# Kernel tuning notes

Measured on AMD Instinct MI355X. Metric: run time of the kernel, lower is better.

Reference implementation:

```python
import jax, jax.numpy as jnp
import numpy as np

N = 100000
DEG = 16
E = N * DEG
IN_DIM = 256
HID = 64
OUT = 64


def setup_inputs() -> dict:
    key = jax.random.key(0)
    ks = jax.random.split(key, 6)
    x = jax.random.normal(ks[0], (N, IN_DIM), dtype=jnp.float32)
    # CSR with fixed degree DEG: row i owns edges [i*DEG, (i+1)*DEG)
    row_id = jnp.repeat(jnp.arange(N, dtype=jnp.int64), DEG)
    col_id = jax.random.randint(ks[1], (E,), 0, N, dtype=jnp.int64)
    adj = jnp.stack([col_id, row_id])  # adj[0]=col, adj[1]=row (matches torch forward)
    row_ptr = (jnp.arange(N + 1, dtype=jnp.int64) * DEG)
    W1 = jax.random.normal(ks[2], (IN_DIM, HID), dtype=jnp.float32) / np.sqrt(IN_DIM)
    b1 = jnp.zeros((HID,), dtype=jnp.float32)
    W2 = jax.random.normal(ks[3], (HID, OUT), dtype=jnp.float32) / np.sqrt(HID)
    b2 = jnp.zeros((OUT,), dtype=jnp.float32)
    return {"x": x, "adj": adj, "row_ptr": row_ptr, "W1": W1, "b1": b1, "W2": W2, "b2": b2}


def agnn_layer(x, row, col, beta):
    # x: [N, d]; row/col: [E]. AGNN: e_ij = beta*cos(x_i, x_j), row-softmax, aggregate x_j.
    norm = jnp.maximum(jnp.linalg.norm(x, axis=-1, keepdims=True), 1e-12)
    xn = x / norm  # [N, d]
    e = beta * jnp.sum(xn[row] * xn[col], axis=-1)  # [E] cosine scores
    # numerically stable segment softmax over rows
    m = jax.ops.segment_max(e, row, num_segments=N)  # [N]
    ex = jnp.exp(e - m[row])  # [E]
    denom = jax.ops.segment_sum(ex, row, num_segments=N)  # [N]
    alpha = ex / jnp.maximum(denom[row], 1e-12)  # [E]
    out = jax.ops.segment_sum(alpha[:, None] * x[col], row, num_segments=N)  # [N, d]
    return out


def reference(x, adj, row_ptr, W1, b1, W2, b2):
    col, row = adj[0], adj[1]
    beta = jnp.float32(1.0)  # non-trainable buffer, initialized to ones
    h = jax.nn.relu(x @ W1 + b1)
    for _ in range(4):
        h = jax.nn.relu(agnn_layer(h, row, col, beta))
    return h @ W2 + b2
```

## Files before the change

kernel.cpp:

```cpp
#include <hip/hip_runtime.h>
#include <math.h>

#define N_NODES 100000
#define DEG 16
#define IN_DIM 256
#define HID 64

typedef _Float16 f16x8 __attribute__((ext_vector_type(8)));
typedef __fp16 fp16x2b __attribute__((ext_vector_type(2)));
typedef float f32x4 __attribute__((ext_vector_type(4)));

union F16x8u {
  f16x8 v;
  fp16x2b h2[4];
};

#if __has_builtin(__builtin_amdgcn_fdot2)
__device__ __forceinline__ float fdot2(fp16x2b a, fp16x2b b, float c) {
  return __builtin_amdgcn_fdot2(a, b, c, false);
}
#else
__device__ __forceinline__ float fdot2(fp16x2b a, fp16x2b b, float c) {
  return fmaf((float)a[0], (float)b[0], fmaf((float)a[1], (float)b[1], c));
}
#endif

__global__ __launch_bounds__(256) void extract_col_kernel(const int* __restrict__ adj,
                                                          int* __restrict__ col, int E) {
  const bool is64 = (adj[2 * E - 1] == 0);
  for (int e = blockIdx.x * blockDim.x + threadIdx.x; e < E; e += gridDim.x * blockDim.x) {
    col[e] = is64 ? adj[2 * e] : adj[e];
  }
}

__global__ __launch_bounds__(256) void prep_wfrag_kernel(const float* __restrict__ W,
                                                         _Float16* __restrict__ wfrag,
                                                         int nfrag) {
  const int id = blockIdx.x * 256 + threadIdx.x;
  if (id >= nfrag) return;
  const int lane = id & 63;
  const int nt = (id >> 6) & 3;
  const int kt = id >> 8;
  const int k0 = kt * 32 + (lane >> 4) * 8;
  const int c = nt * 16 + (lane & 15);
  f16x8 v;
#pragma unroll
  for (int j = 0; j < 8; ++j) v[j] = (_Float16)W[(k0 + j) * HID + c];
  ((f16x8*)wfrag)[id] = v;
}

__global__ __launch_bounds__(256) void mlp1_kernel(const float* __restrict__ x,
                                                   const _Float16* __restrict__ wfrag,
                                                   const float* __restrict__ b1,
                                                   _Float16* __restrict__ hn,
                                                   float* __restrict__ nrm) {
  __shared__ f16x8 Bs[2048];
#pragma unroll
  for (int i = 0; i < 8; ++i)
    Bs[threadIdx.x + 256 * i] = ((const f16x8*)wfrag)[threadIdx.x + 256 * i];

  const int lane = threadIdx.x & 63;
  const int wv = threadIdx.x >> 6;
  const int rbase = blockIdx.x * 64 + wv * 16;
  const int arow = min(rbase + (lane & 15), N_NODES - 1);
  const int kgrp = lane >> 4;
  const float* xrow = x + (size_t)arow * IN_DIM + kgrp * 8;

  f32x4 acc[4];
#pragma unroll
  for (int nt = 0; nt < 4; ++nt) acc[nt] = {0.0f, 0.0f, 0.0f, 0.0f};

  __syncthreads();

#pragma unroll
  for (int kt = 0; kt < 8; ++kt) {
    const float4 a0 = *(const float4*)&xrow[kt * 32];
    const float4 a1 = *(const float4*)&xrow[kt * 32 + 4];
    F16x8u u;
    u.h2[0] = __builtin_amdgcn_cvt_pkrtz(a0.x, a0.y);
    u.h2[1] = __builtin_amdgcn_cvt_pkrtz(a0.z, a0.w);
    u.h2[2] = __builtin_amdgcn_cvt_pkrtz(a1.x, a1.y);
    u.h2[3] = __builtin_amdgcn_cvt_pkrtz(a1.z, a1.w);
#pragma unroll
    for (int nt = 0; nt < 4; ++nt)
      acc[nt] = __builtin_amdgcn_mfma_f32_16x16x32_f16(u.v, Bs[(kt * 4 + nt) * 64 + lane],
                                                       acc[nt], 0, 0, 0);
  }

  const int colb = lane & 15;
  float bias[4];
#pragma unroll
  for (int nt = 0; nt < 4; ++nt) bias[nt] = b1[nt * 16 + colb];

#pragma unroll
  for (int j = 0; j < 4; ++j) {
    float o[4];
#pragma unroll
    for (int nt = 0; nt < 4; ++nt) o[nt] = fmaxf(acc[nt][j] + bias[nt], 0.0f);
    float ss = o[0] * o[0] + o[1] * o[1] + o[2] * o[2] + o[3] * o[3];
    ss += __shfl_xor(ss, 1); ss += __shfl_xor(ss, 2);
    ss += __shfl_xor(ss, 4); ss += __shfl_xor(ss, 8);
    const float nv = sqrtf(ss);
    const float inv = 1.0f / fmaxf(nv, 1e-12f);
    const int row = rbase + kgrp * 4 + j;
    if (row < N_NODES) {
#pragma unroll
      for (int nt = 0; nt < 4; ++nt)
        hn[(size_t)row * HID + nt * 16 + colb] = (_Float16)(o[nt] * inv);
      if (colb == 0) nrm[row] = nv;
    }
  }
}

__global__ __launch_bounds__(256) void agnn_kernel(const _Float16* __restrict__ hn,
                                                   const float* __restrict__ nrm,
                                                   const int* __restrict__ col,
                                                   _Float16* __restrict__ hn_out,
                                                   float* __restrict__ nrm_out) {
  const int lane = threadIdx.x & 63;
  const int wv = threadIdx.x >> 6;
  const int g = lane >> 3;
  const int q = lane & 7;
  const int node = blockIdx.x * 32 + wv * 8 + g;

  const f16x8* hp8 = (const f16x8*)hn;
  F16x8u xi;
  xi.v = hp8[(size_t)node * 8 + q];

  const int cidx0 = col[node * DEG + q];
  const int cidx1 = col[node * DEG + 8 + q];
  const float ncv0 = nrm[cidx0];
  const float ncv1 = nrm[cidx1];

  const int base = (lane & 56) * 4;

  float o[8];
#pragma unroll
  for (int d = 0; d < 8; ++d) o[d] = 0.0f;
  float dn = 0.0f;

#pragma unroll
  for (int c = 0; c < 2; ++c) {
    const int cs = c ? cidx1 : cidx0;
    const float ncv = c ? ncv1 : ncv0;

    F16x8u xcv[8];
#pragma unroll
    for (int k = 0; k < 8; ++k) {
      const int ce = __builtin_amdgcn_ds_bpermute(base + k * 4, cs);
      xcv[k].v = hp8[(size_t)((uint)ce) * 8u + (uint)q];
    }

    float t[8];
#pragma unroll
    for (int k = 0; k < 8; ++k) {
      float s = 0.0f;
#pragma unroll
      for (int j = 0; j < 4; ++j) s = fdot2(xi.h2[j], xcv[k].h2[j], s);
      t[k] = s;
    }

    const bool b0 = (lane & 1), b1 = (lane & 2), b2 = (lane & 4);
    float u[4];
#pragma unroll
    for (int j = 0; j < 4; ++j) {
      const float keep = b0 ? t[2 * j + 1] : t[2 * j];
      const float send = b0 ? t[2 * j] : t[2 * j + 1];
      u[j] = keep + __shfl_xor(send, 1);
    }
    float v[2];
#pragma unroll
    for (int j = 0; j < 2; ++j) {
      const float keep = b1 ? u[2 * j + 1] : u[2 * j];
      const float send = b1 ? u[2 * j] : u[2 * j + 1];
      v[j] = keep + __shfl_xor(send, 2);
    }
    float p;
    {
      const float keep = b2 ? v[1] : v[0];
      const float send = b2 ? v[0] : v[1];
      p = keep + __shfl_xor(send, 4);
    }

    const float ex = __expf(p);
    dn += ex;
    const float wgt = ex * ncv;

#pragma unroll
    for (int k = 0; k < 8; ++k) {
      const float wk = __int_as_float(
          __builtin_amdgcn_ds_bpermute(base + k * 4, __float_as_int(wgt)));
#pragma unroll
      for (int j = 0; j < 4; ++j) {
        o[2 * j] = fmaf((float)xcv[k].h2[j][0], wk, o[2 * j]);
        o[2 * j + 1] = fmaf((float)xcv[k].h2[j][1], wk, o[2 * j + 1]);
      }
    }
  }

  dn += __shfl_xor(dn, 1);
  dn += __shfl_xor(dn, 2);
  dn += __shfl_xor(dn, 4);
  const float idn = 1.0f / dn;

  float ss = 0.0f;
#pragma unroll
  for (int d = 0; d < 8; ++d) {
    o[d] = fmaxf(o[d] * idn, 0.0f);
    ss = fmaf(o[d], o[d], ss);
  }
  ss += __shfl_xor(ss, 1);
  ss += __shfl_xor(ss, 2);
  ss += __shfl_xor(ss, 4);
  const float nv = sqrtf(ss);
  const float inv = 1.0f / fmaxf(nv, 1e-12f);

  F16x8u ov;
#pragma unroll
  for (int d = 0; d < 8; ++d) ov.v[d] = (_Float16)(o[d] * inv);
  ((f16x8*)hn_out)[(size_t)node * 8 + q] = ov.v;
  if (q == 0) nrm_out[node] = nv;
}

__global__ __launch_bounds__(256) void mlp2_kernel(const _Float16* __restrict__ hn,
                                                   const float* __restrict__ nrm,
                                                   const _Float16* __restrict__ w2frag,
                                                   const float* __restrict__ b2,
                                                   float* __restrict__ out) {
  __shared__ f16x8 Bs[512];
  if (threadIdx.x < 256) {
    Bs[threadIdx.x] = ((const f16x8*)w2frag)[threadIdx.x];
    Bs[threadIdx.x + 256] = ((const f16x8*)w2frag)[threadIdx.x + 256];
  }

  const int lane = threadIdx.x & 63;
  const int wv = threadIdx.x >> 6;
  const int rbase = blockIdx.x * 64 + wv * 16;
  const int arow = min(rbase + (lane & 15), N_NODES - 1);
  const int kgrp = lane >> 4;
  const _Float16* hrow = hn + (size_t)arow * HID + kgrp * 8;

  f32x4 acc[4];
#pragma unroll
  for (int nt = 0; nt < 4; ++nt) acc[nt] = {0.0f, 0.0f, 0.0f, 0.0f};

  __syncthreads();

#pragma unroll
  for (int kt = 0; kt < 2; ++kt) {
    const f16x8 a = *(const f16x8*)&hrow[kt * 32];
#pragma unroll
    for (int nt = 0; nt < 4; ++nt)
      acc[nt] = __builtin_amdgcn_mfma_f32_16x16x32_f16(a, Bs[(kt * 4 + nt) * 64 + lane],
                                                       acc[nt], 0, 0, 0);
  }

  const int colb = lane & 15;
  float bias[4];
#pragma unroll
  for (int nt = 0; nt < 4; ++nt) bias[nt] = b2[nt * 16 + colb];

#pragma unroll
  for (int j = 0; j < 4; ++j) {
    const int row = rbase + kgrp * 4 + j;
    const float rnv = nrm[min(row, N_NODES - 1)];
    if (row < N_NODES) {
#pragma unroll
      for (int nt = 0; nt < 4; ++nt)
        out[(size_t)row * HID + nt * 16 + colb] = fmaf(acc[nt][j], rnv, bias[nt]);
    }
  }
}

extern "C" void kernel_launch(void* const* d_in, const int* in_sizes, int n_in,
                              void* d_out, int out_size, void* d_ws, size_t ws_size,
                              hipStream_t stream) {
  const float* x = (const float*)d_in[0];
  const int* adj = (const int*)d_in[1];
  const float* W1 = (const float*)d_in[3];
  const float* b1 = (const float*)d_in[4];
  const float* W2 = (const float*)d_in[5];
  const float* b2 = (const float*)d_in[6];
  float* out = (float*)d_out;

  const int E = N_NODES * DEG;

  char* ws = (char*)d_ws;
  int* col = (int*)ws;
  ws += (size_t)E * sizeof(int);
  _Float16* wfrag = (_Float16*)ws;
  ws += (size_t)IN_DIM * HID * sizeof(_Float16);
  _Float16* w2frag = (_Float16*)ws;
  ws += (size_t)HID * HID * sizeof(_Float16);
  _Float16* hnA = (_Float16*)ws;
  ws += (size_t)N_NODES * HID * sizeof(_Float16);
  _Float16* hnB = (_Float16*)ws;
  ws += (size_t)N_NODES * HID * sizeof(_Float16);
  float* nrA = (float*)ws;
  ws += (size_t)N_NODES * sizeof(float);
  float* nrB = (float*)ws;

  hipLaunchKernelGGL(extract_col_kernel, dim3(2048), dim3(256), 0, stream, adj, col, E);
  hipLaunchKernelGGL(prep_wfrag_kernel, dim3(8), dim3(256), 0, stream, W1, wfrag, 2048);
  hipLaunchKernelGGL(prep_wfrag_kernel, dim3(2), dim3(256), 0, stream, W2, w2frag, 512);

  const int mlp_blocks = (N_NODES + 63) / 64;
  hipLaunchKernelGGL(mlp1_kernel, dim3(mlp_blocks), dim3(256), 0, stream, x, wfrag, b1, hnA, nrA);

  const int agnn_blocks = N_NODES / 32;
  hipLaunchKernelGGL(agnn_kernel, dim3(agnn_blocks), dim3(256), 0, stream, hnA, nrA, col, hnB, nrB);
  hipLaunchKernelGGL(agnn_kernel, dim3(agnn_blocks), dim3(256), 0, stream, hnB, nrB, col, hnA, nrA);
  hipLaunchKernelGGL(agnn_kernel, dim3(agnn_blocks), dim3(256), 0, stream, hnA, nrA, col, hnB, nrB);
  hipLaunchKernelGGL(agnn_kernel, dim3(agnn_blocks), dim3(256), 0, stream, hnB, nrB, col, hnA, nrA);

  hipLaunchKernelGGL(mlp2_kernel, dim3(mlp_blocks), dim3(256), 0, stream, hnA, nrA, w2frag, b2, out);
}
```

Baseline: 159.2 us.

## Store unnormalized features and recompute norms on the fly in AGNN

Node features become unnormalized fp16 activations with no separate norm array. Each AGNN layer now computes the self norm and every neighbor's squared norm from the gathered vectors with extra dot products and shuffle reductions, and scales the cosine score by both reciprocal square roots. This removes the scattered per-neighbor norm gathers and the norm writes and reads across all kernels. The cost is more ALU and shuffle work per edge, and fp16 storage of unnormalized values may change precision or overflow behaviour.

```diff
diff --git a/kernel.cpp b/kernel.cpp
--- a/kernel.cpp
+++ b/kernel.cpp
@@ -52,8 +52,7 @@
 __global__ __launch_bounds__(256) void mlp1_kernel(const float* __restrict__ x,
                                                    const _Float16* __restrict__ wfrag,
                                                    const float* __restrict__ b1,
-                                                   _Float16* __restrict__ hn,
-                                                   float* __restrict__ nrm) {
+                                                   _Float16* __restrict__ h) {
   __shared__ f16x8 Bs[2048];
 #pragma unroll
   for (int i = 0; i < 8; ++i)
@@ -94,43 +93,38 @@
 
 #pragma unroll
   for (int j = 0; j < 4; ++j) {
-    float o[4];
-#pragma unroll
-    for (int nt = 0; nt < 4; ++nt) o[nt] = fmaxf(acc[nt][j] + bias[nt], 0.0f);
-    float ss = o[0] * o[0] + o[1] * o[1] + o[2] * o[2] + o[3] * o[3];
-    ss += __shfl_xor(ss, 1); ss += __shfl_xor(ss, 2);
-    ss += __shfl_xor(ss, 4); ss += __shfl_xor(ss, 8);
-    const float nv = sqrtf(ss);
-    const float inv = 1.0f / fmaxf(nv, 1e-12f);
     const int row = rbase + kgrp * 4 + j;
     if (row < N_NODES) {
 #pragma unroll
       for (int nt = 0; nt < 4; ++nt)
-        hn[(size_t)row * HID + nt * 16 + colb] = (_Float16)(o[nt] * inv);
-      if (colb == 0) nrm[row] = nv;
-    }
-  }
-}
-
-__global__ __launch_bounds__(256) void agnn_kernel(const _Float16* __restrict__ hn,
-                                                   const float* __restrict__ nrm,
+        h[(size_t)row * HID + nt * 16 + colb] =
+            (_Float16)fmaxf(acc[nt][j] + bias[nt], 0.0f);
+    }
+  }
+}
+
+__global__ __launch_bounds__(256) void agnn_kernel(const _Float16* __restrict__ h,
                                                    const int* __restrict__ col,
-                                                   _Float16* __restrict__ hn_out,
-                                                   float* __restrict__ nrm_out) {
+                                                   _Float16* __restrict__ h_out) {
   const int lane = threadIdx.x & 63;
   const int wv = threadIdx.x >> 6;
-  const int g = lane >> 3;
   const int q = lane & 7;
-  const int node = blockIdx.x * 32 + wv * 8 + g;
-
-  const f16x8* hp8 = (const f16x8*)hn;
+  const int node = blockIdx.x * 32 + wv * 8 + (lane >> 3);
+
+  const f16x8* hp8 = (const f16x8*)h;
   F16x8u xi;
   xi.v = hp8[(size_t)node * 8 + q];
 
+  float ssi = 0.0f;
+#pragma unroll
+  for (int j = 0; j < 4; ++j) ssi = fdot2(xi.h2[j], xi.h2[j], ssi);
+  ssi += __shfl_xor(ssi, 1);
+  ssi += __shfl_xor(ssi, 2);
+  ssi += __shfl_xor(ssi, 4);
+  const float ninv_i = rsqrtf(fmaxf(ssi, 1e-24f));
+
   const int cidx0 = col[node * DEG + q];
   const int cidx1 = col[node * DEG + 8 + q];
-  const float ncv0 = nrm[cidx0];
-  const float ncv1 = nrm[cidx1];
 
   const int base = (lane & 56) * 4;
 
@@ -142,7 +136,6 @@
 #pragma unroll
   for (int c = 0; c < 2; ++c) {
     const int cs = c ? cidx1 : cidx0;
-    const float ncv = c ? ncv1 : ncv0;
 
     F16x8u xcv[8];
 #pragma unroll
@@ -151,45 +144,58 @@
       xcv[k].v = hp8[(size_t)((uint)ce) * 8u + (uint)q];
     }
 
-    float t[8];
+    float t[8], s2[8];
 #pragma unroll
     for (int k = 0; k < 8; ++k) {
-      float s = 0.0f;
-#pragma unroll
-      for (int j = 0; j < 4; ++j) s = fdot2(xi.h2[j], xcv[k].h2[j], s);
+      float s = 0.0f, r = 0.0f;
+#pragma unroll
+      for (int j = 0; j < 4; ++j) {
+        s = fdot2(xi.h2[j], xcv[k].h2[j], s);
+        r = fdot2(xcv[k].h2[j], xcv[k].h2[j], r);
+      }
       t[k] = s;
-    }
-
-    const bool b0 = (lane & 1), b1 = (lane & 2), b2 = (lane & 4);
-    float u[4];
+      s2[k] = r;
+    }
+
+    const bool b0 = (lane & 1), b1v = (lane & 2), b2v = (lane & 4);
+    float u[4], ru[4];
 #pragma unroll
     for (int j = 0; j < 4; ++j) {
-      const float keep = b0 ? t[2 * j + 1] : t[2 * j];
-      const float send = b0 ? t[2 * j] : t[2 * j + 1];
-      u[j] = keep + __shfl_xor(send, 1);
-    }
-    float v[2];
+      const float tk = b0 ? t[2 * j + 1] : t[2 * j];
+      const float ts = b0 ? t[2 * j] : t[2 * j + 1];
+      u[j] = tk + __shfl_xor(ts, 1);
+      const float rk = b0 ? s2[2 * j + 1] : s2[2 * j];
+      const float rs = b0 ? s2[2 * j] : s2[2 * j + 1];
+      ru[j] = rk + __shfl_xor(rs, 1);
+    }
+    float v[2], rv[2];
 #pragma unroll
     for (int j = 0; j < 2; ++j) {
-      const float keep = b1 ? u[2 * j + 1] : u[2 * j];
-      const float send = b1 ? u[2 * j] : u[2 * j + 1];
-      v[j] = keep + __shfl_xor(send, 2);
-    }
-    float p;
+      const float tk = b1v ? u[2 * j + 1] : u[2 * j];
+      const float ts = b1v ? u[2 * j] : u[2 * j + 1];
+      v[j] = tk + __shfl_xor(ts, 2);
+      const float rk = b1v ? ru[2 * j + 1] : ru[2 * j];
+      const float rs = b1v ? ru[2 * j] : ru[2 * j + 1];
+      rv[j] = rk + __shfl_xor(rs, 2);
+    }
+    float p, e2;
     {
-      const float keep = b2 ? v[1] : v[0];
-      const float send = b2 ? v[0] : v[1];
-      p = keep + __shfl_xor(send, 4);
-    }
-
-    const float ex = __expf(p);
+      const float tk = b2v ? v[1] : v[0];
+      const float ts = b2v ? v[0] : v[1];
+      p = tk + __shfl_xor(ts, 4);
+      const float rk = b2v ? rv[1] : rv[0];
+      const float rs = b2v ? rv[0] : rv[1];
+      e2 = rk + __shfl_xor(rs, 4);
+    }
+
+    const float ninv_e = rsqrtf(fmaxf(e2, 1e-24f));
+    const float ex = __expf(p * ninv_i * ninv_e);
     dn += ex;
-    const float wgt = ex * ncv;
 
 #pragma unroll
     for (int k = 0; k < 8; ++k) {
       const float wk = __int_as_float(
-          __builtin_amdgcn_ds_bpermute(base + k * 4, __float_as_int(wgt)));
+          __builtin_amdgcn_ds_bpermute(base + k * 4, __float_as_int(ex)));
 #pragma unroll
       for (int j = 0; j < 4; ++j) {
         o[2 * j] = fmaf((float)xcv[k].h2[j][0], wk, o[2 * j]);
@@ -203,27 +209,13 @@
   dn += __shfl_xor(dn, 4);
   const float idn = 1.0f / dn;
 
-  float ss = 0.0f;
-#pragma unroll
-  for (int d = 0; d < 8; ++d) {
-    o[d] = fmaxf(o[d] * idn, 0.0f);
-    ss = fmaf(o[d], o[d], ss);
-  }
-  ss += __shfl_xor(ss, 1);
-  ss += __shfl_xor(ss, 2);
-  ss += __shfl_xor(ss, 4);
-  const float nv = sqrtf(ss);
-  const float inv = 1.0f / fmaxf(nv, 1e-12f);
-
   F16x8u ov;
 #pragma unroll
-  for (int d = 0; d < 8; ++d) ov.v[d] = (_Float16)(o[d] * inv);
-  ((f16x8*)hn_out)[(size_t)node * 8 + q] = ov.v;
-  if (q == 0) nrm_out[node] = nv;
-}
-
-__global__ __launch_bounds__(256) void mlp2_kernel(const _Float16* __restrict__ hn,
-                                                   const float* __restrict__ nrm,
+  for (int d = 0; d < 8; ++d) ov.v[d] = (_Float16)fmaxf(o[d] * idn, 0.0f);
+  ((f16x8*)h_out)[(size_t)node * 8 + q] = ov.v;
+}
+
+__global__ __launch_bounds__(256) void mlp2_kernel(const _Float16* __restrict__ h,
                                                    const _Float16* __restrict__ w2frag,
                                                    const float* __restrict__ b2,
                                                    float* __restrict__ out) {
@@ -238,7 +230,7 @@
   const int rbase = blockIdx.x * 64 + wv * 16;
   const int arow = min(rbase + (lane & 15), N_NODES - 1);
   const int kgrp = lane >> 4;
-  const _Float16* hrow = hn + (size_t)arow * HID + kgrp * 8;
+  const _Float16* hrow = h + (size_t)arow * HID + kgrp * 8;
 
   f32x4 acc[4];
 #pragma unroll
@@ -263,11 +255,10 @@
 #pragma unroll
   for (int j = 0; j < 4; ++j) {
     const int row = rbase + kgrp * 4 + j;
-    const float rnv = nrm[min(row, N_NODES - 1)];
     if (row < N_NODES) {
 #pragma unroll
       for (int nt = 0; nt < 4; ++nt)
-        out[(size_t)row * HID + nt * 16 + colb] = fmaf(acc[nt][j], rnv, bias[nt]);
+        out[(size_t)row * HID + nt * 16 + colb] = acc[nt][j] + bias[nt];
     }
   }
 }
@@ -292,26 +283,22 @@
   ws += (size_t)IN_DIM * HID * sizeof(_Float16);
   _Float16* w2frag = (_Float16*)ws;
   ws += (size_t)HID * HID * sizeof(_Float16);
-  _Float16* hnA = (_Float16*)ws;
+  _Float16* hA = (_Float16*)ws;
   ws += (size_t)N_NODES * HID * sizeof(_Float16);
-  _Float16* hnB = (_Float16*)ws;
-  ws += (size_t)N_NODES * HID * sizeof(_Float16);
-  float* nrA = (float*)ws;
-  ws += (size_t)N_NODES * sizeof(float);
-  float* nrB = (float*)ws;
+  _Float16* hB = (_Float16*)ws;
 
   hipLaunchKernelGGL(extract_col_kernel, dim3(2048), dim3(256), 0, stream, adj, col, E);
   hipLaunchKernelGGL(prep_wfrag_kernel, dim3(8), dim3(256), 0, stream, W1, wfrag, 2048);
   hipLaunchKernelGGL(prep_wfrag_kernel, dim3(2), dim3(256), 0, stream, W2, w2frag, 512);
 
   const int mlp_blocks = (N_NODES + 63) / 64;
-  hipLaunchKernelGGL(mlp1_kernel, dim3(mlp_blocks), dim3(256), 0, stream, x, wfrag, b1, hnA, nrA);
+  hipLaunchKernelGGL(mlp1_kernel, dim3(mlp_blocks), dim3(256), 0, stream, x, wfrag, b1, hA);
 
   const int agnn_blocks = N_NODES / 32;
-  hipLaunchKernelGGL(agnn_kernel, dim3(agnn_blocks), dim3(256), 0, stream, hnA, nrA, col, hnB, nrB);
-  hipLaunchKernelGGL(agnn_kernel, dim3(agnn_blocks), dim3(256), 0, stream, hnB, nrB, col, hnA, nrA);
-  hipLaunchKernelGGL(agnn_kernel, dim3(agnn_blocks), dim3(256), 0, stream, hnA, nrA, col, hnB, nrB);
-  hipLaunchKernelGGL(agnn_kernel, dim3(agnn_blocks), dim3(256), 0, stream, hnB, nrB, col, hnA, nrA);
-
-  hipLaunchKernelGGL(mlp2_kernel, dim3(mlp_blocks), dim3(256), 0, stream, hnA, nrA, w2frag, b2, out);
-}
+  hipLaunchKernelGGL(agnn_kernel, dim3(agnn_blocks), dim3(256), 0, stream, hA, col, hB);
+  hipLaunchKernelGGL(agnn_kernel, dim3(agnn_blocks), dim3(256), 0, stream, hB, col, hA);
+  hipLaunchKernelGGL(agnn_kernel, dim3(agnn_blocks), dim3(256), 0, stream, hA, col, hB);
+  hipLaunchKernelGGL(agnn_kernel, dim3(agnn_blocks), dim3(256), 0, stream, hB, col, hA);
+
+  hipLaunchKernelGGL(mlp2_kernel, dim3(mlp_blocks), dim3(256), 0, stream, hA, w2frag, b2, out);
+}
```

After: 148.9 us. -6.5%, faster.
